# Optimization experiments

Hardware: AMD Instinct MI355X
Metric: run time of the kernel (lower is better)

Reference implementation:

```python
import jax, jax.numpy as jnp
import numpy as np
import math

EMB = 1024
HEADS = 16
B, S = 2, 2048


def setup_inputs() -> dict:
    key = jax.random.key(0)
    k_x, k_wq, k_bq, k_wu, k_bu = jax.random.split(key, 5)
    lim = 1.0 / math.sqrt(EMB)
    x = jax.random.normal(k_x, (B, S, EMB), dtype=jnp.float32)
    # nn.Linear weights: [out, in], uniform(-lim, lim)
    wq = jax.random.uniform(k_wq, (EMB, EMB), jnp.float32, -lim, lim)
    bq = jax.random.uniform(k_bq, (EMB,), jnp.float32, -lim, lim)
    wu = jax.random.uniform(k_wu, (EMB, EMB), jnp.float32, -lim, lim)
    bu = jax.random.uniform(k_bu, (EMB,), jnp.float32, -lim, lim)
    return {"x": x, "wq": wq, "bq": bq, "wu": wu, "bu": bu}


def reference(x, wq, bq, wu, bu):
    b, s, emb = x.shape
    hd = emb // HEADS
    # NOTE: faithful to the original bug — Q, K, V all come from toqueries
    q = jnp.einsum('bse,oe->bso', x, wq) + bq  # [B,S,emb]
    # faithful (buggy) reshape: heads in LEADING dim
    qh = q.reshape(HEADS, b, s, hd)
    kh = qh
    vh = qh
    scale = 1.0 / math.sqrt(emb)  # faithful: sqrt(emb), not sqrt(hd)
    scores = jnp.einsum('hbqd,hbkd->hbqk', qh, kh) * scale  # [H,B,S,S]
    attn = jax.nn.softmax(scores, axis=-1)
    out = jnp.einsum('hbqk,hbkd->hbqd', attn, vh)  # [H,B,S,hd]
    out = out.reshape(b, s, emb)
    return jnp.einsum('bse,oe->bso', out, wu) + bu
```

## Files before the change

### kernel.cpp

```cpp
#include <hip/hip_runtime.h>
#include <stdint.h>

#define EMB 1024
#define HEADS 16
#define NB 2
#define NS 2048
#define HD 64
#define NTOK (NB*NS)
#define KVBLK 64
#define QW 32
#define QBLK 128
#define SEXP2 0.04508421676368185f

typedef __attribute__((ext_vector_type(8))) short short8;
typedef __attribute__((ext_vector_type(4))) float f32x4;
typedef __attribute__((ext_vector_type(4))) unsigned int u32x4;

__device__ inline unsigned short f2bf(float f) {
  unsigned int x = __builtin_bit_cast(unsigned int, f);
  x += 0x7FFFu + ((x >> 16) & 1u);
  return (unsigned short)(x >> 16);
}

__device__ inline unsigned cvt_pk_bf16(float lo, float hi) {
  unsigned d;
  asm("v_cvt_pk_bf16_f32 %0, %1, %2" : "=v"(d) : "v"(lo), "v"(hi));
  return d;
}

__device__ inline void gld16(const void* g, void* l) {
  __builtin_amdgcn_global_load_lds(
      (const __attribute__((address_space(1))) unsigned int*)g,
      (__attribute__((address_space(3))) unsigned int*)l, 16, 0, 0);
}

__global__ void cvt_bf16_kernel(const float* __restrict__ s,
                                unsigned short* __restrict__ d, int n) {
  int i = (blockIdx.x * blockDim.x + threadIdx.x) * 8;
  if (i >= n) return;
  float4 v0 = *reinterpret_cast<const float4*>(s + i);
  float4 v1 = *reinterpret_cast<const float4*>(s + i + 4);
  short8 o;
  o[0] = (short)f2bf(v0.x); o[1] = (short)f2bf(v0.y);
  o[2] = (short)f2bf(v0.z); o[3] = (short)f2bf(v0.w);
  o[4] = (short)f2bf(v1.x); o[5] = (short)f2bf(v1.y);
  o[6] = (short)f2bf(v1.z); o[7] = (short)f2bf(v1.w);
  *reinterpret_cast<short8*>(d + i) = o;
}

__global__ __launch_bounds__(256) void transpose_kernel(
    const unsigned short* __restrict__ src, unsigned short* __restrict__ dst) {
  __shared__ unsigned short t[64][72];
  const int slab = blockIdx.y, kt = blockIdx.x;
  const unsigned short* s = src + ((size_t)slab * NS + kt * 64) * HD;
  unsigned short* d = dst + (size_t)slab * HD * NS + kt * 64;
  const int tid = threadIdx.x;
  #pragma unroll
  for (int c = 0; c < 2; ++c) {
    int idx = c * 256 + tid;
    int row = idx >> 3, col = (idx & 7) * 8;
    short8 v = *reinterpret_cast<const short8*>(s + row * HD + col);
    *reinterpret_cast<short8*>(&t[row][col]) = v;
  }
  __syncthreads();
  #pragma unroll
  for (int c = 0; c < 2; ++c) {
    int idx = c * 256 + tid;
    int drow = idx >> 3, col = (idx & 7) * 8;
    short8 v;
    #pragma unroll
    for (int j = 0; j < 8; ++j) {
      int p = col + j;
      int kv = (p & 32) | (((p >> 2) & 1) << 4) | (((p >> 3) & 3) << 2) | (p & 3);
      v[j] = t[kv][drow];
    }
    *reinterpret_cast<short8*>(d + (size_t)drow * NS + col) = v;
  }
}

template<bool OUT_BF16>
__global__ __launch_bounds__(256) void gemm_bt_kernel(
    const unsigned short* __restrict__ A,
    const unsigned short* __restrict__ Bw,
    const float* __restrict__ bias,
    void* __restrict__ Cout,
    unsigned short* __restrict__ Qscaled,
    int M, int N, int K) {
  __shared__ __align__(16) unsigned short As[2][64 * 64];
  __shared__ __align__(16) unsigned short Bs[2][128 * 64];
  const int tid = threadIdx.x;
  const int lane = tid & 63;
  const int wave = tid >> 6;
  const int wr = wave >> 1, wc = wave & 1;
  const int g = lane >> 4, r = lane & 15;
  const int brow = blockIdx.y * 64;
  const int bcol = blockIdx.x * 128;

  const f32x4 zf = {0.f, 0.f, 0.f, 0.f};
  f32x4 acc[2][4];
  #pragma unroll
  for (int m = 0; m < 2; ++m)
    #pragma unroll
    for (int n = 0; n < 4; ++n) acc[m][n] = zf;

  auto stage = [&](int bb, int k0) {
    #pragma unroll
    for (int i = 0; i < 2; ++i) {
      int base = i * 4096 + wave * 1024;
      int L = base + lane * 16;
      int row = L >> 7, lsl = ((L >> 4) & 7) ^ (row & 7);
      gld16((const char*)A + ((size_t)(brow + row) * K + k0) * 2 + lsl * 16,
            (char*)&As[bb][0] + base);
    }
    #pragma unroll
    for (int i = 0; i < 4; ++i) {
      int base = i * 4096 + wave * 1024;
      int L = base + lane * 16;
      int row = L >> 7, lsl = ((L >> 4) & 7) ^ (row & 7);
      gld16((const char*)Bw + ((size_t)(bcol + row) * K + k0) * 2 + lsl * 16,
            (char*)&Bs[bb][0] + base);
    }
  };

  stage(0, 0);
  int cur = 0;
  for (int k0 = 0; k0 < K; k0 += 64) {
    __syncthreads();
    if (k0 + 64 < K) stage(cur ^ 1, k0 + 64);
    const char* Ac = (const char*)&As[cur][0];
    const char* Bc = (const char*)&Bs[cur][0];
    short8 af[2][2], bfr[4][2];
    #pragma unroll
    for (int m = 0; m < 2; ++m) {
      int row = wr * 32 + m * 16 + r;
      #pragma unroll
      for (int kk = 0; kk < 2; ++kk)
        af[m][kk] = *reinterpret_cast<const short8*>(
            Ac + row * 128 + ((kk * 64 + g * 16) ^ ((row & 7) << 4)));
    }
    #pragma unroll
    for (int n = 0; n < 4; ++n) {
      int row = wc * 64 + n * 16 + r;
      #pragma unroll
      for (int kk = 0; kk < 2; ++kk)
        bfr[n][kk] = *reinterpret_cast<const short8*>(
            Bc + row * 128 + ((kk * 64 + g * 16) ^ ((row & 7) << 4)));
    }
    #pragma unroll
    for (int kk = 0; kk < 2; ++kk)
      #pragma unroll
      for (int m = 0; m < 2; ++m)
        #pragma unroll
        for (int n = 0; n < 4; ++n)
          acc[m][n] = __builtin_amdgcn_mfma_f32_16x16x32_bf16(af[m][kk], bfr[n][kk], acc[m][n], 0, 0, 0);
    cur ^= 1;
  }

  #pragma unroll
  for (int n = 0; n < 4; ++n) {
    int col = bcol + wc * 64 + n * 16 + r;
    float bv = bias[col];
    #pragma unroll
    for (int m = 0; m < 2; ++m) {
      #pragma unroll
      for (int reg = 0; reg < 4; ++reg) {
        int row = brow + wr * 32 + m * 16 + g * 4 + reg;
        float v = acc[m][n][reg] + bv;
        if (OUT_BF16)
          ((unsigned short*)Cout)[(size_t)row * N + col] = f2bf(v);
        else
          ((float*)Cout)[(size_t)row * N + col] = v;
        if (Qscaled)
          Qscaled[(size_t)row * N + col] = f2bf(v * SEXP2);
      }
    }
  }
}

__global__ __launch_bounds__(256) void attn_kernel(
    const unsigned short* __restrict__ qb,
    const unsigned short* __restrict__ qsb,
    const unsigned short* __restrict__ vtb,
    unsigned short* __restrict__ ob) {
  const int bid = blockIdx.x;
  const int xcd = bid & 7, idx = bid >> 3;
  const int slab = xcd * 4 + (idx >> 4);
  const int qtile = idx & 15;
  const unsigned short* Qs = qb + (size_t)slab * NS * HD;
  const unsigned short* Qss = qsb + (size_t)slab * NS * HD;
  const unsigned short* Vts = vtb + (size_t)slab * HD * NS;
  unsigned short* Os = ob + (size_t)slab * NS * HD;
  const int tid = threadIdx.x;
  const int lane = tid & 63;
  const int wave = tid >> 6;
  const int g = lane >> 4, r = lane & 15;
  const int qrow0 = qtile * QBLK + wave * QW;
  const int rkey = (r & 7) << 4;

  __shared__ __align__(16) unsigned short K_lds[2][KVBLK * HD];
  __shared__ __align__(16) unsigned short Vt_lds[2][HD * KVBLK];

  auto stage = [&](int bb, int kt) {
    const char* Kg = (const char*)(Qs + (size_t)kt * KVBLK * HD);
    const char* Vg = (const char*)Vts + (size_t)kt * 128;
    #pragma unroll
    for (int i = 0; i < 2; ++i) {
      int base = i * 4096 + wave * 1024;
      int L = base + lane * 16;
      int row = L >> 7, lsl = ((L >> 4) & 7) ^ (row & 7);
      gld16(Kg + row * 128 + lsl * 16, (char*)&K_lds[bb][0] + base);
      gld16(Vg + (size_t)row * (NS * 2) + lsl * 16, (char*)&Vt_lds[bb][0] + base);
    }
  };

  short8 aq[2][2];
  #pragma unroll
  for (int m = 0; m < 2; ++m)
    #pragma unroll
    for (int kk = 0; kk < 2; ++kk)
      aq[m][kk] = *reinterpret_cast<const short8*>(
          &Qss[(size_t)(qrow0 + m * 16 + r) * HD + kk * 32 + g * 8]);

  const f32x4 zf = {0.f, 0.f, 0.f, 0.f};
  f32x4 o_acc[2][4];
  float l_lane[2] = {0.f, 0.f};
  #pragma unroll
  for (int m = 0; m < 2; ++m)
    #pragma unroll
    for (int n = 0; n < 4; ++n) o_acc[m][n] = zf;

  stage(0, 0);
  int cur = 0;
  for (int kt = 0; kt < NS / KVBLK; ++kt) {
    __syncthreads();
    if (kt + 1 < NS / KVBLK) stage(cur ^ 1, kt + 1);
    const char* Kc = (const char*)&K_lds[cur][0];
    const char* Vc = (const char*)&Vt_lds[cur][0];

    f32x4 s[2][4];
    #pragma unroll
    for (int jb = 0; jb < 4; ++jb) {
      short8 bk[2];
      #pragma unroll
      for (int kk = 0; kk < 2; ++kk)
        bk[kk] = *reinterpret_cast<const short8*>(
            Kc + (jb * 16 + r) * 128 + ((kk * 64 + g * 16) ^ rkey));
      #pragma unroll
      for (int m = 0; m < 2; ++m) {
        s[m][jb] = zf;
        #pragma unroll
        for (int kk = 0; kk < 2; ++kk)
          s[m][jb] = __builtin_amdgcn_mfma_f32_16x16x32_bf16(bk[kk], aq[m][kk], s[m][jb], 0, 0, 0);
      }
    }

    short8 ap[2][2];
    #pragma unroll
    for (int m = 0; m < 2; ++m) {
      float p[4][4];
      #pragma unroll
      for (int jb = 0; jb < 4; ++jb)
        #pragma unroll
        for (int reg = 0; reg < 4; ++reg)
          p[jb][reg] = __builtin_amdgcn_exp2f(s[m][jb][reg]);
      float t0 = (p[0][0] + p[0][1]) + (p[0][2] + p[0][3]);
      float t1 = (p[1][0] + p[1][1]) + (p[1][2] + p[1][3]);
      float t2 = (p[2][0] + p[2][1]) + (p[2][2] + p[2][3]);
      float t3 = (p[3][0] + p[3][1]) + (p[3][2] + p[3][3]);
      l_lane[m] += (t0 + t1) + (t2 + t3);
      #pragma unroll
      for (int kk = 0; kk < 2; ++kk) {
        u32x4 w;
        w.x = cvt_pk_bf16(p[2 * kk][0], p[2 * kk][1]);
        w.y = cvt_pk_bf16(p[2 * kk][2], p[2 * kk][3]);
        w.z = cvt_pk_bf16(p[2 * kk + 1][0], p[2 * kk + 1][1]);
        w.w = cvt_pk_bf16(p[2 * kk + 1][2], p[2 * kk + 1][3]);
        ap[m][kk] = __builtin_bit_cast(short8, w);
      }
    }

    #pragma unroll
    for (int n = 0; n < 4; ++n) {
      short8 bv[2];
      #pragma unroll
      for (int kk = 0; kk < 2; ++kk)
        bv[kk] = *reinterpret_cast<const short8*>(
            Vc + (n * 16 + r) * 128 + ((kk * 64 + g * 16) ^ rkey));
      #pragma unroll
      for (int m = 0; m < 2; ++m)
        #pragma unroll
        for (int kk = 0; kk < 2; ++kk)
          o_acc[m][n] = __builtin_amdgcn_mfma_f32_16x16x32_bf16(ap[m][kk], bv[kk], o_acc[m][n], 0, 0, 0);
    }
    cur ^= 1;
  }

  #pragma unroll
  for (int m = 0; m < 2; ++m) {
    float l = l_lane[m];
    l += __shfl_xor(l, 16);
    l += __shfl_xor(l, 32);
    #pragma unroll
    for (int reg = 0; reg < 4; ++reg) {
      float inv = 1.f / __shfl(l, g * 4 + reg);
      int row = qrow0 + m * 16 + g * 4 + reg;
      #pragma unroll
      for (int n = 0; n < 4; ++n)
        Os[(size_t)row * HD + n * 16 + r] = f2bf(o_acc[m][n][reg] * inv);
    }
  }
}

extern "C" void kernel_launch(void* const* d_in, const int* in_sizes, int n_in,
                              void* d_out, int out_size, void* d_ws, size_t ws_size,
                              hipStream_t stream) {
  const float* x  = (const float*)d_in[0];
  const float* wq = (const float*)d_in[1];
  const float* bq = (const float*)d_in[2];
  const float* wu = (const float*)d_in[3];
  const float* bu = (const float*)d_in[4];
  float* out = (float*)d_out;

  char* ws = (char*)d_ws;
  unsigned short* xb  = (unsigned short*)(ws);
  unsigned short* qb  = (unsigned short*)(ws + (8u  << 20));
  unsigned short* ob  = (unsigned short*)(ws + (16u << 20));
  unsigned short* wqb = (unsigned short*)(ws + (24u << 20));
  unsigned short* wub = (unsigned short*)(ws + (26u << 20));

  cvt_bf16_kernel<<<(NTOK * EMB / 8 + 255) / 256, 256, 0, stream>>>(x, xb, NTOK * EMB);
  cvt_bf16_kernel<<<(EMB * EMB / 8 + 255) / 256, 256, 0, stream>>>(wq, wqb, EMB * EMB);
  cvt_bf16_kernel<<<(EMB * EMB / 8 + 255) / 256, 256, 0, stream>>>(wu, wub, EMB * EMB);

  unsigned short* qsb = ob;
  gemm_bt_kernel<true><<<dim3(EMB / 128, NTOK / 64), 256, 0, stream>>>(
      xb, wqb, bq, qb, qsb, NTOK, EMB, EMB);

  unsigned short* vtb = xb;
  transpose_kernel<<<dim3(NS / 64, HEADS * NB), 256, 0, stream>>>(qb, vtb);

  attn_kernel<<<dim3(512), 256, 0, stream>>>(qb, qsb, vtb, ob);

  gemm_bt_kernel<false><<<dim3(EMB / 128, NTOK / 64), 256, 0, stream>>>(
      ob, wub, bu, out, (unsigned short*)nullptr, NTOK, EMB, EMB);
}
```

Measured before the change: 108.7 us.

## Shrink GEMM and attention tiles, fuse weight casts, use explicit waitcnt barriers

The GEMM tile drops from 64x128 to 64x64 and the attention block from 4 waves to 2 waves over 64 query rows, which doubles the grid sizes to 1024 blocks to fill more CUs. The two weight-cast launches are merged into one kernel. The attention loop swaps __syncthreads for explicit s_barrier plus vmcnt waits, so the next KV tile's loads stay in flight during compute. Smaller tiles mean more redundant K/V and weight traffic per output element.

```diff
diff --git a/kernel.cpp b/kernel.cpp
--- a/kernel.cpp
+++ b/kernel.cpp
@@ -8,8 +8,6 @@
 #define HD 64
 #define NTOK (NB*NS)
 #define KVBLK 64
-#define QW 32
-#define QBLK 128
 #define SEXP2 0.04508421676368185f
 
 typedef __attribute__((ext_vector_type(8))) short short8;
@@ -48,6 +46,25 @@
   *reinterpret_cast<short8*>(d + i) = o;
 }
 
+__global__ void cvt_bf16x2_kernel(const float* __restrict__ s0,
+                                  unsigned short* __restrict__ d0,
+                                  const float* __restrict__ s1,
+                                  unsigned short* __restrict__ d1, int n0, int n1) {
+  int i = (blockIdx.x * blockDim.x + threadIdx.x) * 8;
+  const float* s; unsigned short* d;
+  if (i < n0) { s = s0 + i; d = d0 + i; }
+  else if (i - n0 < n1) { s = s1 + (i - n0); d = d1 + (i - n0); }
+  else return;
+  float4 v0 = *reinterpret_cast<const float4*>(s);
+  float4 v1 = *reinterpret_cast<const float4*>(s + 4);
+  short8 o;
+  o[0] = (short)f2bf(v0.x); o[1] = (short)f2bf(v0.y);
+  o[2] = (short)f2bf(v0.z); o[3] = (short)f2bf(v0.w);
+  o[4] = (short)f2bf(v1.x); o[5] = (short)f2bf(v1.y);
+  o[6] = (short)f2bf(v1.z); o[7] = (short)f2bf(v1.w);
+  *reinterpret_cast<short8*>(d) = o;
+}
+
 __global__ __launch_bounds__(256) void transpose_kernel(
     const unsigned short* __restrict__ src, unsigned short* __restrict__ dst) {
   __shared__ unsigned short t[64][72];
@@ -87,21 +104,21 @@
     unsigned short* __restrict__ Qscaled,
     int M, int N, int K) {
   __shared__ __align__(16) unsigned short As[2][64 * 64];
-  __shared__ __align__(16) unsigned short Bs[2][128 * 64];
+  __shared__ __align__(16) unsigned short Bs[2][64 * 64];
   const int tid = threadIdx.x;
   const int lane = tid & 63;
   const int wave = tid >> 6;
   const int wr = wave >> 1, wc = wave & 1;
   const int g = lane >> 4, r = lane & 15;
   const int brow = blockIdx.y * 64;
-  const int bcol = blockIdx.x * 128;
+  const int bcol = blockIdx.x * 64;
 
   const f32x4 zf = {0.f, 0.f, 0.f, 0.f};
-  f32x4 acc[2][4];
+  f32x4 acc[2][2];
   #pragma unroll
   for (int m = 0; m < 2; ++m)
     #pragma unroll
-    for (int n = 0; n < 4; ++n) acc[m][n] = zf;
+    for (int n = 0; n < 2; ++n) acc[m][n] = zf;
 
   auto stage = [&](int bb, int k0) {
     #pragma unroll
@@ -113,7 +130,7 @@
             (char*)&As[bb][0] + base);
     }
     #pragma unroll
-    for (int i = 0; i < 4; ++i) {
+    for (int i = 0; i < 2; ++i) {
       int base = i * 4096 + wave * 1024;
       int L = base + lane * 16;
       int row = L >> 7, lsl = ((L >> 4) & 7) ^ (row & 7);
@@ -129,7 +146,7 @@
     if (k0 + 64 < K) stage(cur ^ 1, k0 + 64);
     const char* Ac = (const char*)&As[cur][0];
     const char* Bc = (const char*)&Bs[cur][0];
-    short8 af[2][2], bfr[4][2];
+    short8 af[2][2], bfr[2][2];
     #pragma unroll
     for (int m = 0; m < 2; ++m) {
       int row = wr * 32 + m * 16 + r;
@@ -139,8 +156,8 @@
             Ac + row * 128 + ((kk * 64 + g * 16) ^ ((row & 7) << 4)));
     }
     #pragma unroll
-    for (int n = 0; n < 4; ++n) {
-      int row = wc * 64 + n * 16 + r;
+    for (int n = 0; n < 2; ++n) {
+      int row = wc * 32 + n * 16 + r;
       #pragma unroll
       for (int kk = 0; kk < 2; ++kk)
         bfr[n][kk] = *reinterpret_cast<const short8*>(
@@ -151,14 +168,14 @@
       #pragma unroll
       for (int m = 0; m < 2; ++m)
         #pragma unroll
-        for (int n = 0; n < 4; ++n)
+        for (int n = 0; n < 2; ++n)
           acc[m][n] = __builtin_amdgcn_mfma_f32_16x16x32_bf16(af[m][kk], bfr[n][kk], acc[m][n], 0, 0, 0);
     cur ^= 1;
   }
 
   #pragma unroll
-  for (int n = 0; n < 4; ++n) {
-    int col = bcol + wc * 64 + n * 16 + r;
+  for (int n = 0; n < 2; ++n) {
+    int col = bcol + wc * 32 + n * 16 + r;
     float bv = bias[col];
     #pragma unroll
     for (int m = 0; m < 2; ++m) {
@@ -177,15 +194,15 @@
   }
 }
 
-__global__ __launch_bounds__(256) void attn_kernel(
+__global__ __launch_bounds__(128) void attn_kernel(
     const unsigned short* __restrict__ qb,
     const unsigned short* __restrict__ qsb,
     const unsigned short* __restrict__ vtb,
     unsigned short* __restrict__ ob) {
   const int bid = blockIdx.x;
   const int xcd = bid & 7, idx = bid >> 3;
-  const int slab = xcd * 4 + (idx >> 4);
-  const int qtile = idx & 15;
+  const int slab = xcd * 4 + (idx >> 5);
+  const int qtile = idx & 31;
   const unsigned short* Qs = qb + (size_t)slab * NS * HD;
   const unsigned short* Qss = qsb + (size_t)slab * NS * HD;
   const unsigned short* Vts = vtb + (size_t)slab * HD * NS;
@@ -194,7 +211,7 @@
   const int lane = tid & 63;
   const int wave = tid >> 6;
   const int g = lane >> 4, r = lane & 15;
-  const int qrow0 = qtile * QBLK + wave * QW;
+  const int qrow0 = qtile * 64 + wave * 32;
   const int rkey = (r & 7) << 4;
 
   __shared__ __align__(16) unsigned short K_lds[2][KVBLK * HD];
@@ -204,8 +221,8 @@
     const char* Kg = (const char*)(Qs + (size_t)kt * KVBLK * HD);
     const char* Vg = (const char*)Vts + (size_t)kt * 128;
     #pragma unroll
-    for (int i = 0; i < 2; ++i) {
-      int base = i * 4096 + wave * 1024;
+    for (int i = 0; i < 4; ++i) {
+      int base = (i * 2 + wave) * 1024;
       int L = base + lane * 16;
       int row = L >> 7, lsl = ((L >> 4) & 7) ^ (row & 7);
       gld16(Kg + row * 128 + lsl * 16, (char*)&K_lds[bb][0] + base);
@@ -220,6 +237,7 @@
     for (int kk = 0; kk < 2; ++kk)
       aq[m][kk] = *reinterpret_cast<const short8*>(
           &Qss[(size_t)(qrow0 + m * 16 + r) * HD + kk * 32 + g * 8]);
+  asm volatile("s_waitcnt vmcnt(0)" ::: "memory");
 
   const f32x4 zf = {0.f, 0.f, 0.f, 0.f};
   f32x4 o_acc[2][4];
@@ -232,8 +250,16 @@
   stage(0, 0);
   int cur = 0;
   for (int kt = 0; kt < NS / KVBLK; ++kt) {
-    __syncthreads();
-    if (kt + 1 < NS / KVBLK) stage(cur ^ 1, kt + 1);
+    __builtin_amdgcn_s_barrier();
+    if (kt + 1 < NS / KVBLK) {
+      stage(cur ^ 1, kt + 1);
+      asm volatile("s_waitcnt vmcnt(8)" ::: "memory");
+    } else {
+      asm volatile("s_waitcnt vmcnt(0)" ::: "memory");
+    }
+    __builtin_amdgcn_s_barrier();
+    __builtin_amdgcn_sched_barrier(0);
+
     const char* Kc = (const char*)&K_lds[cur][0];
     const char* Vc = (const char*)&Vt_lds[cur][0];
 
@@ -329,18 +355,18 @@
   unsigned short* wub = (unsigned short*)(ws + (26u << 20));
 
   cvt_bf16_kernel<<<(NTOK * EMB / 8 + 255) / 256, 256, 0, stream>>>(x, xb, NTOK * EMB);
-  cvt_bf16_kernel<<<(EMB * EMB / 8 + 255) / 256, 256, 0, stream>>>(wq, wqb, EMB * EMB);
-  cvt_bf16_kernel<<<(EMB * EMB / 8 + 255) / 256, 256, 0, stream>>>(wu, wub, EMB * EMB);
+  cvt_bf16x2_kernel<<<(2 * EMB * EMB / 8 + 255) / 256, 256, 0, stream>>>(
+      wq, wqb, wu, wub, EMB * EMB, EMB * EMB);
 
   unsigned short* qsb = ob;
-  gemm_bt_kernel<true><<<dim3(EMB / 128, NTOK / 64), 256, 0, stream>>>(
+  gemm_bt_kernel<true><<<dim3(EMB / 64, NTOK / 64), 256, 0, stream>>>(
       xb, wqb, bq, qb, qsb, NTOK, EMB, EMB);
 
   unsigned short* vtb = xb;
   transpose_kernel<<<dim3(NS / 64, HEADS * NB), 256, 0, stream>>>(qb, vtb);
 
-  attn_kernel<<<dim3(512), 256, 0, stream>>>(qb, qsb, vtb, ob);
-
-  gemm_bt_kernel<false><<<dim3(EMB / 128, NTOK / 64), 256, 0, stream>>>(
+  attn_kernel<<<dim3(1024), 128, 0, stream>>>(qb, qsb, vtb, ob);
+
+  gemm_bt_kernel<false><<<dim3(EMB / 64, NTOK / 64), 256, 0, stream>>>(
       ob, wub, bu, out, (unsigned short*)nullptr, NTOK, EMB, EMB);
 }
```

New measurement: 107.4 us. No clear change (-1.2%).
